# Kernel optimization log

Measured on AMD Instinct MI355X. Metric: run time of the kernel, lower is better.

## Reference

```python
import jax, jax.numpy as jnp
import numpy as np
from jax import lax

DIM = 64        # Branch(dim)
OUT = 2048      # TimesBlock out_channels == TTT model_dim
NH = 8          # num_heads
HD = OUT // NH  # 256 head dim
INNER = 4 * HD  # ttt_mlp hidden
MB = 10         # mini_batch_size
BASE_LR = 0.1   # ttt_base_lr
NK = 6          # TimesBlock num_kernels (k = 1,3,5,7,9,11)
LN_EPS = 1e-6


def _gelu(x):
    return jax.nn.gelu(x, approximate=False)


def _gelu_bwd(x):
    return 0.5 * (1.0 + lax.erf(x / jnp.sqrt(2.0))) + x * jnp.exp(-0.5 * x * x) / jnp.sqrt(2.0 * jnp.pi)


def _ttt_head(qs, ks, vs, W1h, b1h, W2h, b2h, gw, gb):
    # qs/ks/vs: [NC, MB, HD]; sequential scan over mini-batch chunks (TTT inner GD)
    eta = BASE_LR / MB

    def step(carry, chunk):
        W1c, b1c, W2c, b2c = carry
        xq, xk, xv = chunk
        Z1 = xk @ W1c + b1c              # [MB, INNER]
        A1 = _gelu(Z1)
        Z2 = A1 @ W2c + b2c              # [MB, HD]
        # grad of 0.5*||LN(Z2) - (xv - xk)||^2 wrt Z2 (fused LN l2 backward)
        tgt = xv - xk
        mu = Z2.mean(-1, keepdims=True)
        std = jnp.sqrt(Z2.var(-1, keepdims=True) + LN_EPS)
        xhat = (2 * 0 + Z2 - mu) / std
        gout = (gw * xhat + gb) - tgt
        gxh = gout * gw
        gZ2 = (gxh - gxh.mean(-1, keepdims=True) - xhat * (gxh * xhat).mean(-1, keepdims=True)) / std
        gZ1 = (gZ2 @ W2c.T) * _gelu_bwd(Z1)
        # inner-model SGD step
        W1n = W1c - eta * (xk.T @ gZ1)
        b1n = b1c - eta * gZ1.sum(0)
        W2n = W2c - eta * (A1.T @ gZ2)
        b2n = b2c - eta * gZ2.sum(0)
        # apply updated inner model to queries, post-LN + residual
        Z1q = xq @ W1n + b1n
        Z2q = _gelu(Z1q) @ W2n + b2n
        muq = Z2q.mean(-1, keepdims=True)
        stdq = jnp.sqrt(Z2q.var(-1, keepdims=True) + LN_EPS)
        out = xq + gw * ((Z2q - muq) / stdq) + gb
        return (W1n, b1n, W2n, b2n), out

    _, outs = lax.scan(step, (W1h, b1h, W2h, b2h), (qs, ks, vs))
    return outs.reshape(-1, HD)  # [T, HD]


def _forward(x, seg, conv_ws, conv_bs, wq, wk, wv, wo, W1, b1, W2, b2, ln_w, ln_b):
    B, T, C = x.shape
    xg = jnp.transpose(x, (0, 2, 1)).reshape(B, C, T // seg, seg)
    dn = ('NCHW', 'OIHW', 'NCHW')
    acc = 0.0
    for w, bc in zip(conv_ws, conv_bs):
        acc = acc + lax.conv_general_dilated(xg, w, (1, 1), 'SAME', dimension_numbers=dn) + bc[None, :, None, None]
    xb = acc / float(len(conv_ws))            # TimesBlock: mean over kernel ensemble
    xb = jax.nn.silu(xb)
    xb = jnp.transpose(xb.reshape(B, OUT, T), (0, 2, 1))  # [B, T, OUT]

    def heads(h):  # [B,T,OUT] -> [B,NH,NC,MB,HD]
        return jnp.transpose(h.reshape(B, T, NH, HD), (0, 2, 1, 3)).reshape(B, NH, T // MB, MB, HD)

    q = heads(xb @ wq.T)
    k = heads(xb @ wk.T)
    v = heads(xb @ wv.T)
    f = jax.vmap(jax.vmap(_ttt_head, in_axes=(0, 0, 0, 0, 0, 0, 0, 0, 0)),
                 in_axes=(0, 0, 0, None, None, None, None, None, None))
    o = f(q, k, v, W1, b1, W2, b2, ln_w, ln_b)  # [B, NH, T, HD]
    o = jnp.transpose(o, (0, 2, 1, 3)).reshape(B, T, OUT)
    return o @ wo.T


def setup_inputs() -> dict:
    key = jax.random.key(0)
    ks = jax.random.split(key, 24)
    B, T = 2, 400
    inp = {"x": jax.random.normal(ks[0], (B, T, DIM), jnp.float32), "seg": 20}
    for i in range(NK):
        kk = 2 * i + 1
        fan_out = OUT * kk * kk
        inp[f"conv_w{i}"] = jax.random.normal(ks[1 + i], (OUT, DIM, kk, kk), jnp.float32) * np.sqrt(2.0 / fan_out)
        inp[f"conv_b{i}"] = jnp.zeros((OUT,), jnp.float32)
    for j, nm in enumerate(["wq", "wk", "wv", "wo"]):
        inp[nm] = jax.random.normal(ks[8 + j], (OUT, OUT), jnp.float32) * 0.02
    inp["W1"] = jax.random.normal(ks[12], (NH, HD, INNER), jnp.float32) * 0.02
    inp["b1"] = jnp.zeros((NH, INNER), jnp.float32)
    inp["W2"] = jax.random.normal(ks[13], (NH, INNER, HD), jnp.float32) * 0.02
    inp["b2"] = jnp.zeros((NH, HD), jnp.float32)
    inp["ln_w"] = jnp.ones((NH, HD), jnp.float32)
    inp["ln_b"] = jnp.zeros((NH, HD), jnp.float32)
    return inp


def reference(x, seg, conv_w0, conv_b0, conv_w1, conv_b1, conv_w2, conv_b2,
              conv_w3, conv_b3, conv_w4, conv_b4, conv_w5, conv_b5,
              wq, wk, wv, wo, W1, b1, W2, b2, ln_w, ln_b):
    conv_ws = [conv_w0, conv_w1, conv_w2, conv_w3, conv_w4, conv_w5]
    conv_bs = [conv_b0, conv_b1, conv_b2, conv_b3, conv_b4, conv_b5]
    return _forward(x, seg, conv_ws, conv_bs, wq, wk, wv, wo, W1, b1, W2, b2, ln_w, ln_b)
```

## Files before the change

kernel.cpp:

```cpp
#include <hip/hip_runtime.h>


typedef __bf16 bf16x8 __attribute__((ext_vector_type(8)));
typedef float  f32x4  __attribute__((ext_vector_type(4)));

__device__ __forceinline__ unsigned short f2bf(float f){
  unsigned int u = __builtin_bit_cast(unsigned int, f);
  u += 0x7fffu + ((u >> 16) & 1u);
  return (unsigned short)(u >> 16);
}
__device__ __forceinline__ float bf2f(unsigned short b){
  unsigned int u = ((unsigned int)b) << 16;
  return __builtin_bit_cast(float, u);
}
__device__ __forceinline__ float gelu_f(float x){
  return 0.5f * x * (1.0f + erff(x * 0.70710678118654752f));
}
__device__ __forceinline__ float gelu_bwd_f(float x){
  return 0.5f * (1.0f + erff(x * 0.70710678118654752f))
       + x * __expf(-0.5f * x * x) * 0.3989422804014327f;
}

__device__ __forceinline__ float2 aload2(const float* p){
  unsigned long long v = __hip_atomic_load((const unsigned long long*)p,
                                           __ATOMIC_RELAXED, __HIP_MEMORY_SCOPE_AGENT);
  union { unsigned long long u; float2 f; } cv; cv.u = v; return cv.f;
}
__device__ __forceinline__ void aadd(float* p, float v){
  __hip_atomic_fetch_add(p, v, __ATOMIC_RELAXED, __HIP_MEMORY_SCOPE_AGENT);
}


__global__ __launch_bounds__(256) void k_weff(
    const float* __restrict__ w0, const float* __restrict__ w1,
    const float* __restrict__ w2, const float* __restrict__ w3,
    const float* __restrict__ w4, const float* __restrict__ w5,
    unsigned short* __restrict__ weff)
{
  extern __shared__ float sw[];
  const int off[6] = {0, 64, 640, 2240, 5376, 10560};
  const float* ws6[6] = {w0, w1, w2, w3, w4, w5};
  int o = blockIdx.x, tid = threadIdx.x;
#pragma unroll
  for (int i = 0; i < 6; i++){
    int kk = 2 * i + 1, sz = 64 * kk * kk;
    const float* src = ws6[i] + (size_t)o * sz;
    for (int idx = tid; idx < sz; idx += 256) sw[off[i] + idx] = src[idx];
  }
  __syncthreads();
  for (int t = tid; t < 7744; t += 256){
    int c = t / 121, dd = t % 121, di = dd / 11, dj = dd % 11;
    float s = 0.f;
#pragma unroll
    for (int i = 0; i < 6; i++){
      int kk = 2 * i + 1;
      int a = di - 5 + i, b = dj - 5 + i;
      if (a >= 0 && a < kk && b >= 0 && b < kk)
        s += sw[off[i] + (c * kk + a) * kk + b];
    }
    weff[(size_t)o * 7744 + t] = f2bf(s);
  }
}

__global__ __launch_bounds__(256) void k_im2col(
    const float* __restrict__ x, unsigned short* __restrict__ P)
{
  int idx = blockIdx.x * 256 + threadIdx.x;
  if (idx >= 800 * 7744) return;
  int n = idx / 7744, k = idx % 7744;
  int c = k / 121, dd = k % 121, di = dd / 11, dj = dd % 11;
  int b = n / 400, pos = n % 400, i = pos / 20, j = pos % 20;
  int ii = i + di - 5, jj = j + dj - 5;
  float v = 0.f;
  if (ii >= 0 && ii < 20 && jj >= 0 && jj < 20)
    v = x[((size_t)b * 400 + ii * 20 + jj) * 64 + c];
  P[idx] = f2bf(v);
}

__global__ __launch_bounds__(256) void k_wqkv(
    const float* __restrict__ wq, const float* __restrict__ wk,
    const float* __restrict__ wv, unsigned short* __restrict__ dst)
{
  int idx = blockIdx.x * 256 + threadIdx.x;
  if (idx >= 6144 * 2048) return;
  int m = idx >> 11, kk = idx & 2047;
  const float* src = (m < 2048) ? wq : ((m < 4096) ? wk : wv);
  dst[idx] = f2bf(src[(size_t)(m & 2047) * 2048 + kk]);
}

__global__ __launch_bounds__(256) void k_f2bf_copy(
    const float* __restrict__ src, unsigned short* __restrict__ dst, int n)
{
  int idx = blockIdx.x * 256 + threadIdx.x;
  if (idx < n) dst[idx] = f2bf(src[idx]);
}

__global__ __launch_bounds__(256) void k_bsum(
    const float* __restrict__ b0, const float* __restrict__ b1,
    const float* __restrict__ b2, const float* __restrict__ b3,
    const float* __restrict__ b4, const float* __restrict__ b5,
    float* __restrict__ bsum)
{
  int idx = blockIdx.x * 256 + threadIdx.x;
  if (idx < 2048)
    bsum[idx] = b0[idx] + b1[idx] + b2[idx] + b3[idx] + b4[idx] + b5[idx];
}

__global__ __launch_bounds__(256) void k_comb_silu(
    const float* __restrict__ p0, const float* __restrict__ p1,
    const float* __restrict__ bsum, unsigned short* __restrict__ xb)
{
  int i4 = (blockIdx.x * 256 + threadIdx.x) * 4;
  float4 a = *(const float4*)&p0[i4];
  float4 b = *(const float4*)&p1[i4];
  int mm = i4 & 2047;
  float4 bs = *(const float4*)&bsum[mm];
  float v[4] = {a.x + b.x + bs.x, a.y + b.y + bs.y, a.z + b.z + bs.z, a.w + b.w + bs.w};
  ushort4 o;
#pragma unroll
  for (int i = 0; i < 4; i++){
    float t = v[i] * (1.0f / 6.0f);
    float sv = t / (1.0f + __expf(-t));
    ((unsigned short*)&o)[i] = f2bf(sv);
  }
  *(ushort4*)&xb[i4] = o;
}

__global__ __launch_bounds__(256) void k_comb_add(
    const float* __restrict__ p0, const float* __restrict__ p1,
    float* __restrict__ out)
{
  int i4 = (blockIdx.x * 256 + threadIdx.x) * 4;
  float4 a = *(const float4*)&p0[i4];
  float4 b = *(const float4*)&p1[i4];
  float4 o = {a.x + b.x, a.y + b.y, a.z + b.z, a.w + b.w};
  *(float4*)&out[i4] = o;
}

template<int MODE>
__global__ __launch_bounds__(256, 1) void k_gemm(
    const unsigned short* __restrict__ A, const unsigned short* __restrict__ B,
    int M, int N, int lda, int ldb, int kLen,
    unsigned short* __restrict__ qb, unsigned short* __restrict__ kb,
    unsigned short* __restrict__ vb, float* __restrict__ outf)
{
  __shared__ unsigned short As[128 * 32];
  __shared__ unsigned short Bs[128 * 32];
  int tid = threadIdx.x, w = tid >> 6, l = tid & 63, qd = l >> 4, lm = l & 15;
  int m0 = blockIdx.x * 128, n0 = blockIdx.y * 128;
  int kBase = blockIdx.z * kLen;

  f32x4 acc[4][4];
#pragma unroll
  for (int i = 0; i < 4; i++)
#pragma unroll
    for (int j = 0; j < 4; j++){ acc[i][j][0]=0.f; acc[i][j][1]=0.f; acc[i][j][2]=0.f; acc[i][j][3]=0.f; }

  int nk = kLen >> 5;
  for (int kt = 0; kt < nk; kt++){
    int k0 = kBase + (kt << 5);
#pragma unroll
    for (int i = 0; i < 2; i++){
      int cidx = tid + i * 256;
      int row = cidx >> 2, kc = (cidx & 3) << 3;
      *(uint4*)&As[row * 32 + kc] = *(const uint4*)&A[(size_t)(m0 + row) * lda + k0 + kc];
      int br = n0 + row; if (br >= N) br = N - 1;
      *(uint4*)&Bs[row * 32 + kc] = *(const uint4*)&B[(size_t)br * ldb + k0 + kc];
    }
    __syncthreads();
    bf16x8 af[4], bfv[4];
#pragma unroll
    for (int i = 0; i < 4; i++)
      af[i] = *(const bf16x8*)&As[((w >> 1) * 64 + i * 16 + lm) * 32 + qd * 8];
#pragma unroll
    for (int j = 0; j < 4; j++)
      bfv[j] = *(const bf16x8*)&Bs[((w & 1) * 64 + j * 16 + lm) * 32 + qd * 8];
#pragma unroll
    for (int i = 0; i < 4; i++)
#pragma unroll
      for (int j = 0; j < 4; j++)
        acc[i][j] = __builtin_amdgcn_mfma_f32_16x16x32_bf16(af[i], bfv[j], acc[i][j], 0, 0, 0);
    __syncthreads();
  }

#pragma unroll
  for (int i = 0; i < 4; i++){
    int mBase = m0 + (w >> 1) * 64 + i * 16 + qd * 4;
#pragma unroll
    for (int j = 0; j < 4; j++){
      int n = n0 + (w & 1) * 64 + j * 16 + lm;
      if (n < N){
#pragma unroll
        for (int rr = 0; rr < 4; rr++){
          float val = acc[i][j][rr];
          int mm = mBase + rr;
          if (MODE == 1){
            int proj = mm >> 11, o = mm & 2047, hh = o >> 8, d = o & 255;
            int bh = (n / 400) * 8 + hh, tt = n % 400;
            unsigned short* dst = (proj == 0) ? qb : ((proj == 1) ? kb : vb);
            dst[((size_t)bh * 400 + tt) * 256 + d] = f2bf(val);
          } else {
            outf[(size_t)blockIdx.z * M * N + (size_t)n * M + mm] = val;
          }
        }
      }
    }
  }
}

#define O_W1BT 0
#define O_W2K  16896
#define O_W2N  33792
#define O_XKQ  52224
#define O_TGT  54864
#define O_A1   57424
#define O_A1T  58144
#define O_GZ2  60704
#define O_GZ1  63344
#define O_XQ2  65392
#define O_GZ2T 68032
#define O_XKT  74176
#define O_F32  80320
#define O_GW   80960
#define O_GB   81216
#define US_TOTAL 81472
#define TTT_LDS_BYTES (81472 * 2)

#define ETA 0.01f
#define BAR_STRIDE 32

__global__ __launch_bounds__(256, 1) void k_ttt(
    const unsigned short* __restrict__ qg, const unsigned short* __restrict__ kg,
    const unsigned short* __restrict__ vg,
    const float* __restrict__ W1g, const float* __restrict__ b1g,
    const float* __restrict__ W2g, const float* __restrict__ b2g,
    const float* __restrict__ gwg, const float* __restrict__ gbg,
    float* __restrict__ z2acc, unsigned short* __restrict__ zqp,
    unsigned int* __restrict__ bar)
{
  extern __shared__ unsigned short lds[];
  float* ldsf = (float*)&lds[O_F32];

  int tid = threadIdx.x, w = tid >> 6, l = tid & 63, qd = l >> 4, lm = l & 15;
  int bid = blockIdx.x;
  int jj = bid >> 3, xx = bid & 7;
  int h  = xx + 8 * (jj >> 4);
  int sl = jj & 15;
  int hh = h & 7;

  for (int i = tid; i < US_TOTAL; i += 256) lds[i] = 0;
  __syncthreads();

  float w1r[4][4][4];
#pragma unroll
  for (int a = 0; a < 4; a++)
#pragma unroll
    for (int nt = 0; nt < 4; nt++)
#pragma unroll
      for (int rr = 0; rr < 4; rr++)
        w1r[a][nt][rr] = W1g[((size_t)hh * 256 + (4 * w + a) * 16 + qd * 4 + rr) * 1024
                             + sl * 64 + nt * 16 + lm];
  float w2r[16][4];
#pragma unroll
  for (int nt = 0; nt < 16; nt++)
#pragma unroll
    for (int rr = 0; rr < 4; rr++)
      w2r[nt][rr] = W2g[((size_t)hh * 1024 + sl * 64 + w * 16 + qd * 4 + rr) * 256
                        + nt * 16 + lm];
  if (tid < 64)  ldsf[tid] = b1g[hh * 1024 + sl * 64 + tid];
  if (tid < 256){
    ldsf[64 + tid] = b2g[hh * 256 + tid];
    lds[O_GW + tid] = f2bf(gwg[hh * 256 + tid]);
    lds[O_GB + tid] = f2bf(gbg[hh * 256 + tid]);
  }

#define WRITE_W1BF() do { \
  _Pragma("unroll") for (int a = 0; a < 4; a++){ \
    int m0i = (4 * w + a) * 16 + qd * 4; \
    _Pragma("unroll") for (int nt = 0; nt < 4; nt++){ \
      int n = nt * 16 + lm; \
      unsigned int p0 = f2bf(w1r[a][nt][0]) | ((unsigned int)f2bf(w1r[a][nt][1]) << 16); \
      unsigned int p1 = f2bf(w1r[a][nt][2]) | ((unsigned int)f2bf(w1r[a][nt][3]) << 16); \
      *(unsigned int*)&lds[O_W1BT + n * 264 + m0i]     = p0; \
      *(unsigned int*)&lds[O_W1BT + n * 264 + m0i + 2] = p1; \
    } } } while(0)

#define WRITE_W2BF() do { \
  int mB = w * 16 + qd * 4; \
  _Pragma("unroll") for (int nt = 0; nt < 16; nt++){ \
    int n = nt * 16 + lm; \
    _Pragma("unroll") for (int rr = 0; rr < 4; rr++) \
      lds[O_W2K + (mB + rr) * 264 + n] = f2bf(w2r[nt][rr]); \
    unsigned int p0 = f2bf(w2r[nt][0]) | ((unsigned int)f2bf(w2r[nt][1]) << 16); \
    unsigned int p1 = f2bf(w2r[nt][2]) | ((unsigned int)f2bf(w2r[nt][3]) << 16); \
    *(unsigned int*)&lds[O_W2N + n * 72 + mB]     = p0; \
    *(unsigned int*)&lds[O_W2N + n * 72 + mB + 2] = p1; \
  } } while(0)

  const size_t hb2 = (size_t)h * 400 * 256;

#define LOAD_XK_TGT(NCH) do { \
  const unsigned int* kp = (const unsigned int*)(kg + hb2 + (size_t)(NCH) * 2560); \
  const unsigned int* vp = (const unsigned int*)(vg + hb2 + (size_t)(NCH) * 2560); \
  _Pragma("unroll") for (int i5 = 0; i5 < 5; i5++){ \
    int f2i = i5 * 256 + tid; \
    unsigned int ku = kp[f2i], vu = vp[f2i]; \
    int row = f2i >> 7, col = (f2i & 127) * 2; \
    *(unsigned int*)&lds[O_XKQ + row * 264 + col] = ku; \
    lds[O_XKT + col * 24 + row]       = (unsigned short)(ku & 0xffffu); \
    lds[O_XKT + (col + 1) * 24 + row] = (unsigned short)(ku >> 16); \
    float kv0 = bf2f((unsigned short)(ku & 0xffffu)), kv1 = bf2f((unsigned short)(ku >> 16)); \
    float vv0 = bf2f((unsigned short)(vu & 0xffffu)), vv1 = bf2f((unsigned short)(vu >> 16)); \
    unsigned int tu = (unsigned int)f2bf(vv0 - kv0) | ((unsigned int)f2bf(vv1 - kv1) << 16); \
    *(unsigned int*)&lds[O_TGT + row * 256 + col] = tu; \
  } } while(0)

  WRITE_W1BF();
  WRITE_W2BF();
  LOAD_XK_TGT(0);
  __syncthreads();

  for (int nch = 0; nch < 40; nch++){
    const size_t chunkBase = (size_t)(h * 40 + nch) * 10 * 256;

    f32x4 z1a; z1a[0]=0.f; z1a[1]=0.f; z1a[2]=0.f; z1a[3]=0.f;
#pragma unroll
    for (int ks = 0; ks < 8; ks++){
      bf16x8 av = *(const bf16x8*)&lds[O_XKQ + lm * 264 + ks * 32 + qd * 8];
      bf16x8 bv = *(const bf16x8*)&lds[O_W1BT + (w * 16 + lm) * 264 + ks * 32 + qd * 8];
      z1a = __builtin_amdgcn_mfma_f32_16x16x32_bf16(av, bv, z1a, 0, 0, 0);
    }
    float z1v[4];
    {
      float b1n = ldsf[w * 16 + lm];
#pragma unroll
      for (int rr = 0; rr < 4; rr++){
        z1v[rr] = z1a[rr] + b1n;
        int mr = qd * 4 + rr;
        if (mr < 10){
          float a1 = gelu_f(z1v[rr]);
          unsigned short ab = f2bf(a1);
          lds[O_A1 + mr * 72 + w * 16 + lm] = ab;
          lds[O_A1T + (w * 16 + lm) * 40 + mr] = ab;
        }
      }
    }
    __syncthreads();

#pragma unroll
    for (int nt4 = 0; nt4 < 4; nt4++){
      int nt = 4 * w + nt4;
      f32x4 p; p[0]=0.f; p[1]=0.f; p[2]=0.f; p[3]=0.f;
#pragma unroll
      for (int ks = 0; ks < 2; ks++){
        bf16x8 av = *(const bf16x8*)&lds[O_A1 + lm * 72 + ks * 32 + qd * 8];
        bf16x8 bv = *(const bf16x8*)&lds[O_W2N + (nt * 16 + lm) * 72 + ks * 32 + qd * 8];
        p = __builtin_amdgcn_mfma_f32_16x16x32_bf16(av, bv, p, 0, 0, 0);
      }
#pragma unroll
      for (int rr = 0; rr < 4; rr++){
        int mr = qd * 4 + rr;
        if (mr < 10)
          aadd(&z2acc[chunkBase + (size_t)mr * 256 + nt * 16 + lm], p[rr]);
      }
    }

    {
      const unsigned int* qp = (const unsigned int*)(qg + hb2 + (size_t)nch * 2560);
#pragma unroll
      for (int i5 = 0; i5 < 5; i5++){
        int f2i = i5 * 256 + tid;
        unsigned int qu = qp[f2i];
        int row = f2i >> 7, col = (f2i & 127) * 2;
        *(unsigned int*)&lds[O_XQ2 + row * 264 + col] = qu;
      }
    }

    __syncthreads();
    if (tid == 0){
      __hip_atomic_fetch_add(bar + h * BAR_STRIDE, 1u, __ATOMIC_RELAXED, __HIP_MEMORY_SCOPE_AGENT);
      unsigned int target = 16u * (unsigned int)(nch + 1);
      unsigned int spins = 0;
      while (__hip_atomic_load(bar + h * BAR_STRIDE, __ATOMIC_RELAXED, __HIP_MEMORY_SCOPE_AGENT) < target
             && spins < 8000000u){ spins++; __builtin_amdgcn_s_sleep(1); }
    }
    __syncthreads();

    for (int r2 = w; r2 < 10; r2 += 4){
      int c0 = l * 4;
      const float* bp = &z2acc[chunkBase + (size_t)r2 * 256 + c0];
      float2 u01 = aload2(bp);
      float2 u23 = aload2(bp + 2);
      float zz[4] = {u01.x, u01.y, u23.x, u23.y};
      float s1 = 0.f, s2 = 0.f;
#pragma unroll
      for (int i = 0; i < 4; i++){ zz[i] += ldsf[64 + c0 + i]; s1 += zz[i]; s2 += zz[i] * zz[i]; }
#pragma unroll
      for (int off = 32; off >= 1; off >>= 1){ s1 += __shfl_xor(s1, off, 64); s2 += __shfl_xor(s2, off, 64); }
      float mu = s1 * (1.f / 256.f);
      float var = s2 * (1.f / 256.f) - mu * mu;
      float rstd = rsqrtf(var + 1e-6f);
      float xh[4], gx[4];
      float t1 = 0.f, t2 = 0.f;
#pragma unroll
      for (int i = 0; i < 4; i++){
        xh[i] = (zz[i] - mu) * rstd;
        float gwv = bf2f(lds[O_GW + c0 + i]), gbv = bf2f(lds[O_GB + c0 + i]);
        float tg = bf2f(lds[O_TGT + r2 * 256 + c0 + i]);
        float go = gwv * xh[i] + gbv - tg;
        gx[i] = go * gwv;
        t1 += gx[i]; t2 += gx[i] * xh[i];
      }
#pragma unroll
      for (int off = 32; off >= 1; off >>= 1){ t1 += __shfl_xor(t1, off, 64); t2 += __shfl_xor(t2, off, 64); }
      float m1 = t1 * (1.f / 256.f), m2 = t2 * (1.f / 256.f);
      float g0 = (gx[0] - m1 - xh[0] * m2) * rstd;
      float g1 = (gx[1] - m1 - xh[1] * m2) * rstd;
      float g2 = (gx[2] - m1 - xh[2] * m2) * rstd;
      float g3 = (gx[3] - m1 - xh[3] * m2) * rstd;
      unsigned int p0 = f2bf(g0) | ((unsigned int)f2bf(g1) << 16);
      unsigned int p1 = f2bf(g2) | ((unsigned int)f2bf(g3) << 16);
      *(unsigned int*)&lds[O_GZ2 + r2 * 264 + c0]     = p0;
      *(unsigned int*)&lds[O_GZ2 + r2 * 264 + c0 + 2] = p1;
    }
    __syncthreads();

    {
      float sum = 0.f;
#pragma unroll
      for (int r2 = 0; r2 < 10; r2++){
        unsigned short g = lds[O_GZ2 + r2 * 264 + tid];
        lds[O_GZ2T + tid * 24 + r2] = g;
        sum += bf2f(g);
      }
      ldsf[64 + tid] -= ETA * sum;
    }
    {
      f32x4 g1a; g1a[0]=0.f; g1a[1]=0.f; g1a[2]=0.f; g1a[3]=0.f;
#pragma unroll
      for (int ks = 0; ks < 8; ks++){
        bf16x8 av = *(const bf16x8*)&lds[O_GZ2 + lm * 264 + ks * 32 + qd * 8];
        bf16x8 bv = *(const bf16x8*)&lds[O_W2K + (w * 16 + lm) * 264 + ks * 32 + qd * 8];
        g1a = __builtin_amdgcn_mfma_f32_16x16x32_bf16(av, bv, g1a, 0, 0, 0);
      }
#pragma unroll
      for (int rr = 0; rr < 4; rr++){
        int mr = qd * 4 + rr;
        if (mr < 10){
          float gz1 = g1a[rr] * gelu_bwd_f(z1v[rr]);
          lds[O_GZ1 + (w * 16 + lm) * 32 + mr] = f2bf(gz1);
        }
      }
    }
    __syncthreads();

    if (tid < 64){
      float sum = 0.f;
#pragma unroll
      for (int kx = 0; kx < 10; kx++) sum += bf2f(lds[O_GZ1 + tid * 32 + kx]);
      ldsf[tid] -= ETA * sum;
    }
#pragma unroll
    for (int a = 0; a < 4; a++){
      int mt = 4 * w + a;
      bf16x8 av = *(const bf16x8*)&lds[O_XKT + (mt * 16 + lm) * 24 + (qd & 1) * 8];
#pragma unroll
      for (int nt = 0; nt < 4; nt++){
        bf16x8 bv = *(const bf16x8*)&lds[O_GZ1 + (nt * 16 + lm) * 32 + qd * 8];
        f32x4 d; d[0]=0.f; d[1]=0.f; d[2]=0.f; d[3]=0.f;
        d = __builtin_amdgcn_mfma_f32_16x16x32_bf16(av, bv, d, 0, 0, 0);
#pragma unroll
        for (int rr = 0; rr < 4; rr++) w1r[a][nt][rr] -= ETA * d[rr];
      }
    }
    {
      bf16x8 av2 = *(const bf16x8*)&lds[O_A1T + (w * 16 + lm) * 40 + qd * 8];
#pragma unroll
      for (int nt = 0; nt < 16; nt++){
        bf16x8 bv = *(const bf16x8*)&lds[O_GZ2T + (nt * 16 + lm) * 24 + (qd & 1) * 8];
        f32x4 d; d[0]=0.f; d[1]=0.f; d[2]=0.f; d[3]=0.f;
        d = __builtin_amdgcn_mfma_f32_16x16x32_bf16(av2, bv, d, 0, 0, 0);
#pragma unroll
        for (int rr = 0; rr < 4; rr++) w2r[nt][rr] -= ETA * d[rr];
      }
    }
    WRITE_W1BF();
    WRITE_W2BF();
    __syncthreads();

    if (nch + 1 < 40) LOAD_XK_TGT(nch + 1);

    {
      f32x4 zq; zq[0]=0.f; zq[1]=0.f; zq[2]=0.f; zq[3]=0.f;
#pragma unroll
      for (int ks = 0; ks < 8; ks++){
        bf16x8 av = *(const bf16x8*)&lds[O_XQ2 + lm * 264 + ks * 32 + qd * 8];
        bf16x8 bv = *(const bf16x8*)&lds[O_W1BT + (w * 16 + lm) * 264 + ks * 32 + qd * 8];
        zq = __builtin_amdgcn_mfma_f32_16x16x32_bf16(av, bv, zq, 0, 0, 0);
      }
      float b1n = ldsf[w * 16 + lm];
#pragma unroll
      for (int rr = 0; rr < 4; rr++){
        int mr = qd * 4 + rr;
        if (mr < 10)
          lds[O_A1 + mr * 72 + w * 16 + lm] = f2bf(gelu_f(zq[rr] + b1n));
      }
    }
    __syncthreads();

    {
      unsigned short* zq_out = zqp + ((size_t)(h * 16 + sl) * 40 + nch) * 2560;
#pragma unroll
      for (int nt4 = 0; nt4 < 4; nt4++){
        int nt = 4 * w + nt4;
        f32x4 p; p[0]=0.f; p[1]=0.f; p[2]=0.f; p[3]=0.f;
#pragma unroll
        for (int ks = 0; ks < 2; ks++){
          bf16x8 av = *(const bf16x8*)&lds[O_A1 + lm * 72 + ks * 32 + qd * 8];
          bf16x8 bv = *(const bf16x8*)&lds[O_W2N + (nt * 16 + lm) * 72 + ks * 32 + qd * 8];
          p = __builtin_amdgcn_mfma_f32_16x16x32_bf16(av, bv, p, 0, 0, 0);
        }
        float bb = (sl == 0) ? ldsf[64 + nt * 16 + lm] : 0.f;
#pragma unroll
        for (int rr = 0; rr < 4; rr++){
          int mr = qd * 4 + rr;
          if (mr < 10)
            zq_out[mr * 256 + nt * 16 + lm] = f2bf(p[rr] + bb);
        }
      }
    }
    __syncthreads();
  }
}

__global__ __launch_bounds__(256) void k_lnout(
    const unsigned short* __restrict__ zqp, const unsigned short* __restrict__ qg,
    const float* __restrict__ gwg, const float* __restrict__ gbg,
    unsigned short* __restrict__ obf)
{
  int w = threadIdx.x >> 6, l = threadIdx.x & 63;
  int gr = blockIdx.x * 4 + w;
  int h = gr / 400, t = gr % 400, hh = h & 7, b = h >> 3;
  int nch = t / 10, mr = t % 10;
  int c0 = l * 4;
  float z[4] = {0.f, 0.f, 0.f, 0.f};
#pragma unroll
  for (int sl = 0; sl < 16; sl++){
    const unsigned short* zp = zqp + (((size_t)(h * 16 + sl) * 40 + nch) * 10 + mr) * 256 + c0;
    ushort4 u = *(const ushort4*)zp;
    z[0] += bf2f(u.x); z[1] += bf2f(u.y); z[2] += bf2f(u.z); z[3] += bf2f(u.w);
  }
  float s1 = 0.f, s2 = 0.f;
#pragma unroll
  for (int i = 0; i < 4; i++){ s1 += z[i]; s2 += z[i] * z[i]; }
#pragma unroll
  for (int off = 32; off >= 1; off >>= 1){ s1 += __shfl_xor(s1, off, 64); s2 += __shfl_xor(s2, off, 64); }
  float mu = s1 * (1.f / 256.f);
  float var = s2 * (1.f / 256.f) - mu * mu;
  float rstd = rsqrtf(var + 1e-6f);
  const unsigned short* qp = &qg[((size_t)h * 400 + t) * 256];
  ushort4 qu = *(const ushort4*)&qp[c0];
  float qv[4] = {bf2f(qu.x), bf2f(qu.y), bf2f(qu.z), bf2f(qu.w)};
  unsigned short* op = &obf[((size_t)(b * 400 + t)) * 2048 + hh * 256];
#pragma unroll
  for (int i = 0; i < 4; i++){
    float xh = (z[i] - mu) * rstd;
    float o = qv[i] + gwg[hh * 256 + c0 + i] * xh + gbg[hh * 256 + c0 + i];
    op[c0 + i] = f2bf(o);
  }
}

#define WS_WEFF   0u
#define WS_P      31719424u
#define WS_WQKV   44109824u
#define WS_WOB    52428800u
#define WS_Z2ACC  62722048u
#define WS_XB     69275648u
#define WS_Q      72552448u
#define WS_K      75829248u
#define WS_V      79106048u
#define WS_OBF    82382848u
#define WS_BSUM   85659648u
#define WS_BAR    85667840u

extern "C" void kernel_launch(void* const* d_in, const int* in_sizes, int n_in,
                              void* d_out, int out_size, void* d_ws, size_t ws_size,
                              hipStream_t stream)
{
  (void)in_sizes; (void)n_in; (void)out_size; (void)ws_size;
  const float* x  = (const float*)d_in[0];
  const float* cw[6]; const float* cb[6];
  for (int i = 0; i < 6; i++){ cw[i] = (const float*)d_in[2 + 2 * i]; cb[i] = (const float*)d_in[3 + 2 * i]; }
  const float* wq  = (const float*)d_in[14];
  const float* wk  = (const float*)d_in[15];
  const float* wv  = (const float*)d_in[16];
  const float* wo  = (const float*)d_in[17];
  const float* W1  = (const float*)d_in[18];
  const float* b1  = (const float*)d_in[19];
  const float* W2  = (const float*)d_in[20];
  const float* b2  = (const float*)d_in[21];
  const float* lnw = (const float*)d_in[22];
  const float* lnb = (const float*)d_in[23];
  float* outf = (float*)d_out;

  char* wsb = (char*)d_ws;
  unsigned short* weff = (unsigned short*)(wsb + WS_WEFF);
  unsigned short* P    = (unsigned short*)(wsb + WS_P);
  unsigned short* wqkv = (unsigned short*)(wsb + WS_WQKV);
  unsigned short* wob  = (unsigned short*)(wsb + WS_WOB);
  unsigned short* xb   = (unsigned short*)(wsb + WS_XB);
  unsigned short* qb   = (unsigned short*)(wsb + WS_Q);
  unsigned short* kb   = (unsigned short*)(wsb + WS_K);
  unsigned short* vb   = (unsigned short*)(wsb + WS_V);
  float* z2acc = (float*)(wsb + WS_Z2ACC);
  unsigned short* zqp = (unsigned short*)(wsb + WS_WEFF);
  unsigned short* obf = (unsigned short*)(wsb + WS_OBF);
  float* bsum = (float*)(wsb + WS_BSUM);
  unsigned int* bar = (unsigned int*)(wsb + WS_BAR);
  float* g0part = (float*)(wsb + WS_Q);
  float* g2part = (float*)(wsb + WS_Z2ACC);

  hipMemsetAsync(bar, 0, 16 * BAR_STRIDE * 4, stream);
  hipFuncSetAttribute(reinterpret_cast<const void*>(k_ttt),
                      hipFuncAttributeMaxDynamicSharedMemorySize, TTT_LDS_BYTES);
  hipFuncSetAttribute(reinterpret_cast<const void*>(k_weff),
                      hipFuncAttributeMaxDynamicSharedMemorySize, 18304 * 4);

  k_weff<<<2048, 256, 18304 * 4, stream>>>(cw[0], cw[1], cw[2], cw[3], cw[4], cw[5], weff);
  k_im2col<<<(800 * 7744 + 255) / 256, 256, 0, stream>>>(x, P);
  k_wqkv<<<(6144 * 2048 + 255) / 256, 256, 0, stream>>>(wq, wk, wv, wqkv);
  k_bsum<<<8, 256, 0, stream>>>(cb[0], cb[1], cb[2], cb[3], cb[4], cb[5], bsum);

  k_gemm<2><<<dim3(16, 7, 2), 256, 0, stream>>>(weff, P, 2048, 800, 7744, 7744, 3872,
                                                nullptr, nullptr, nullptr, g0part);
  k_comb_silu<<<1600, 256, 0, stream>>>(g0part, g0part + 1638400, bsum, xb);

  k_gemm<1><<<dim3(48, 7, 1), 256, 0, stream>>>(wqkv, xb, 6144, 800, 2048, 2048, 2048,
                                                qb, kb, vb, nullptr);

  k_f2bf_copy<<<(2048 * 2048 + 255) / 256, 256, 0, stream>>>(wo, wob, 2048 * 2048);
  hipMemsetAsync(z2acc, 0, 16 * 40 * 10 * 256 * 4, stream);

  k_ttt<<<256, 256, TTT_LDS_BYTES, stream>>>(qb, kb, vb, W1, b1, W2, b2, lnw, lnb,
                                             z2acc, zqp, bar);
  k_lnout<<<1600, 256, 0, stream>>>(zqp, qb, lnw, lnb, obf);

  k_gemm<2><<<dim3(16, 7, 2), 256, 0, stream>>>(wob, obf, 2048, 800, 2048, 2048, 1024,
                                                nullptr, nullptr, nullptr, g2part);
  k_comb_add<<<1600, 256, 0, stream>>>(g2part, g2part + 1638400, outf);
}
```

Baseline: 1.130 ms.

## Overlap deferred query output with cross-block barrier wait; split output GEMM four-way

In the TTT kernel, the query-path output for chunk n-1 (Z1q, GELU and the Z2q MFMA plus the global store) now runs after the barrier arrive and before the spin-wait for chunk n. The wait latency is hidden behind useful work, and the query load for the next chunk is prefetched in the same window, with a tail step after the loop for the last chunk. The A1T LDS stride is shrunk and a separate A1Q buffer is added. The output projection GEMM uses a 4-way K split instead of 2-way for more blocks, and its partials go to a larger workspace region combined by a 4-input add kernel. The risks are extra partial-sum traffic and correctness of the reordered synchronisation.

```diff
diff --git a/kernel.cpp b/kernel.cpp
--- a/kernel.cpp
+++ b/kernel.cpp
@@ -126,14 +126,16 @@
   *(ushort4*)&xb[i4] = o;
 }
 
-__global__ __launch_bounds__(256) void k_comb_add(
-    const float* __restrict__ p0, const float* __restrict__ p1,
-    float* __restrict__ out)
+__global__ __launch_bounds__(256) void k_comb_add4(
+    const float* __restrict__ p, float* __restrict__ out)
 {
   int i4 = (blockIdx.x * 256 + threadIdx.x) * 4;
-  float4 a = *(const float4*)&p0[i4];
-  float4 b = *(const float4*)&p1[i4];
-  float4 o = {a.x + b.x, a.y + b.y, a.z + b.z, a.w + b.w};
+  float4 a = *(const float4*)&p[i4];
+  float4 b = *(const float4*)&p[1638400 + i4];
+  float4 c = *(const float4*)&p[3276800 + i4];
+  float4 d = *(const float4*)&p[4915200 + i4];
+  float4 o = {a.x + b.x + c.x + d.x, a.y + b.y + c.y + d.y,
+              a.z + b.z + c.z + d.z, a.w + b.w + c.w + d.w};
   *(float4*)&out[i4] = o;
 }
 
@@ -215,16 +217,17 @@
 #define O_TGT  54864
 #define O_A1   57424
 #define O_A1T  58144
-#define O_GZ2  60704
-#define O_GZ1  63344
-#define O_XQ2  65392
-#define O_GZ2T 68032
-#define O_XKT  74176
-#define O_F32  80320
-#define O_GW   80960
-#define O_GB   81216
-#define US_TOTAL 81472
-#define TTT_LDS_BYTES (81472 * 2)
+#define O_GZ2  60192
+#define O_GZ1  62832
+#define O_XQ2  64880
+#define O_GZ2T 67520
+#define O_XKT  73664
+#define O_A1Q  79808
+#define O_F32  80528
+#define O_GW   81168
+#define O_GB   81424
+#define US_TOTAL 81680
+#define TTT_LDS_BYTES (81680 * 2)
 
 #define ETA 0.01f
 #define BAR_STRIDE 32
@@ -315,9 +318,19 @@
     *(unsigned int*)&lds[O_TGT + row * 256 + col] = tu; \
   } } while(0)
 
+#define LOAD_XQ(NCH) do { \
+  const unsigned int* qp = (const unsigned int*)(qg + hb2 + (size_t)(NCH) * 2560); \
+  _Pragma("unroll") for (int i5 = 0; i5 < 5; i5++){ \
+    int f2i = i5 * 256 + tid; \
+    unsigned int qu = qp[f2i]; \
+    int row = f2i >> 7, col = (f2i & 127) * 2; \
+    *(unsigned int*)&lds[O_XQ2 + row * 264 + col] = qu; \
+  } } while(0)
+
   WRITE_W1BF();
   WRITE_W2BF();
   LOAD_XK_TGT(0);
+  LOAD_XQ(0);
   __syncthreads();
 
   for (int nch = 0; nch < 40; nch++){
@@ -341,7 +354,7 @@
           float a1 = gelu_f(z1v[rr]);
           unsigned short ab = f2bf(a1);
           lds[O_A1 + mr * 72 + w * 16 + lm] = ab;
-          lds[O_A1T + (w * 16 + lm) * 40 + mr] = ab;
+          lds[O_A1T + (w * 16 + lm) * 32 + mr] = ab;
         }
       }
     }
@@ -364,21 +377,53 @@
           aadd(&z2acc[chunkBase + (size_t)mr * 256 + nt * 16 + lm], p[rr]);
       }
     }
-
-    {
-      const unsigned int* qp = (const unsigned int*)(qg + hb2 + (size_t)nch * 2560);
-#pragma unroll
-      for (int i5 = 0; i5 < 5; i5++){
-        int f2i = i5 * 256 + tid;
-        unsigned int qu = qp[f2i];
-        int row = f2i >> 7, col = (f2i & 127) * 2;
-        *(unsigned int*)&lds[O_XQ2 + row * 264 + col] = qu;
-      }
-    }
-
-    __syncthreads();
+    __syncthreads();
+
+    if (tid == 0)
+      __hip_atomic_fetch_add(bar + h * BAR_STRIDE, 1u, __ATOMIC_RELAXED, __HIP_MEMORY_SCOPE_AGENT);
+
+    if (nch > 0){
+      f32x4 zq; zq[0]=0.f; zq[1]=0.f; zq[2]=0.f; zq[3]=0.f;
+#pragma unroll
+      for (int ks = 0; ks < 8; ks++){
+        bf16x8 av = *(const bf16x8*)&lds[O_XQ2 + lm * 264 + ks * 32 + qd * 8];
+        bf16x8 bv = *(const bf16x8*)&lds[O_W1BT + (w * 16 + lm) * 264 + ks * 32 + qd * 8];
+        zq = __builtin_amdgcn_mfma_f32_16x16x32_bf16(av, bv, zq, 0, 0, 0);
+      }
+      float b1n = ldsf[w * 16 + lm];
+#pragma unroll
+      for (int rr = 0; rr < 4; rr++){
+        int mr = qd * 4 + rr;
+        if (mr < 10)
+          lds[O_A1Q + mr * 72 + w * 16 + lm] = f2bf(gelu_f(zq[rr] + b1n));
+      }
+    }
+    __syncthreads();
+
+    if (nch > 0){
+      LOAD_XQ(nch);
+      unsigned short* zq_out = zqp + ((size_t)(h * 16 + sl) * 40 + (nch - 1)) * 2560;
+#pragma unroll
+      for (int nt4 = 0; nt4 < 4; nt4++){
+        int nt = 4 * w + nt4;
+        f32x4 p; p[0]=0.f; p[1]=0.f; p[2]=0.f; p[3]=0.f;
+#pragma unroll
+        for (int ks = 0; ks < 2; ks++){
+          bf16x8 av = *(const bf16x8*)&lds[O_A1Q + lm * 72 + ks * 32 + qd * 8];
+          bf16x8 bv = *(const bf16x8*)&lds[O_W2N + (nt * 16 + lm) * 72 + ks * 32 + qd * 8];
+          p = __builtin_amdgcn_mfma_f32_16x16x32_bf16(av, bv, p, 0, 0, 0);
+        }
+        float bb = (sl == 0) ? ldsf[64 + nt * 16 + lm] : 0.f;
+#pragma unroll
+        for (int rr = 0; rr < 4; rr++){
+          int mr = qd * 4 + rr;
+          if (mr < 10)
+            zq_out[mr * 256 + nt * 16 + lm] = f2bf(p[rr] + bb);
+        }
+      }
+    }
+
     if (tid == 0){
-      __hip_atomic_fetch_add(bar + h * BAR_STRIDE, 1u, __ATOMIC_RELAXED, __HIP_MEMORY_SCOPE_AGENT);
       unsigned int target = 16u * (unsigned int)(nch + 1);
       unsigned int spins = 0;
       while (__hip_atomic_load(bar + h * BAR_STRIDE, __ATOMIC_RELAXED, __HIP_MEMORY_SCOPE_AGENT) < target
@@ -474,7 +519,7 @@
       }
     }
     {
-      bf16x8 av2 = *(const bf16x8*)&lds[O_A1T + (w * 16 + lm) * 40 + qd * 8];
+      bf16x8 av2 = *(const bf16x8*)&lds[O_A1T + (w * 16 + lm) * 32 + qd * 8];
 #pragma unroll
       for (int nt = 0; nt < 16; nt++){
         bf16x8 bv = *(const bf16x8*)&lds[O_GZ2T + (nt * 16 + lm) * 24 + (qd & 1) * 8];
@@ -488,48 +533,49 @@
     WRITE_W2BF();
     __syncthreads();
 
-    if (nch + 1 < 40) LOAD_XK_TGT(nch + 1);
-
-    {
-      f32x4 zq; zq[0]=0.f; zq[1]=0.f; zq[2]=0.f; zq[3]=0.f;
-#pragma unroll
-      for (int ks = 0; ks < 8; ks++){
-        bf16x8 av = *(const bf16x8*)&lds[O_XQ2 + lm * 264 + ks * 32 + qd * 8];
-        bf16x8 bv = *(const bf16x8*)&lds[O_W1BT + (w * 16 + lm) * 264 + ks * 32 + qd * 8];
-        zq = __builtin_amdgcn_mfma_f32_16x16x32_bf16(av, bv, zq, 0, 0, 0);
-      }
-      float b1n = ldsf[w * 16 + lm];
+    if (nch + 1 < 40){
+      LOAD_XK_TGT(nch + 1);
+    }
+    __syncthreads();
+  }
+
+  {
+    f32x4 zq; zq[0]=0.f; zq[1]=0.f; zq[2]=0.f; zq[3]=0.f;
+#pragma unroll
+    for (int ks = 0; ks < 8; ks++){
+      bf16x8 av = *(const bf16x8*)&lds[O_XQ2 + lm * 264 + ks * 32 + qd * 8];
+      bf16x8 bv = *(const bf16x8*)&lds[O_W1BT + (w * 16 + lm) * 264 + ks * 32 + qd * 8];
+      zq = __builtin_amdgcn_mfma_f32_16x16x32_bf16(av, bv, zq, 0, 0, 0);
+    }
+    float b1n = ldsf[w * 16 + lm];
+#pragma unroll
+    for (int rr = 0; rr < 4; rr++){
+      int mr = qd * 4 + rr;
+      if (mr < 10)
+        lds[O_A1Q + mr * 72 + w * 16 + lm] = f2bf(gelu_f(zq[rr] + b1n));
+    }
+  }
+  __syncthreads();
+  {
+    unsigned short* zq_out = zqp + ((size_t)(h * 16 + sl) * 40 + 39) * 2560;
+#pragma unroll
+    for (int nt4 = 0; nt4 < 4; nt4++){
+      int nt = 4 * w + nt4;
+      f32x4 p; p[0]=0.f; p[1]=0.f; p[2]=0.f; p[3]=0.f;
+#pragma unroll
+      for (int ks = 0; ks < 2; ks++){
+        bf16x8 av = *(const bf16x8*)&lds[O_A1Q + lm * 72 + ks * 32 + qd * 8];
+        bf16x8 bv = *(const bf16x8*)&lds[O_W2N + (nt * 16 + lm) * 72 + ks * 32 + qd * 8];
+        p = __builtin_amdgcn_mfma_f32_16x16x32_bf16(av, bv, p, 0, 0, 0);
+      }
+      float bb = (sl == 0) ? ldsf[64 + nt * 16 + lm] : 0.f;
 #pragma unroll
       for (int rr = 0; rr < 4; rr++){
         int mr = qd * 4 + rr;
         if (mr < 10)
-          lds[O_A1 + mr * 72 + w * 16 + lm] = f2bf(gelu_f(zq[rr] + b1n));
-      }
-    }
-    __syncthreads();
-
-    {
-      unsigned short* zq_out = zqp + ((size_t)(h * 16 + sl) * 40 + nch) * 2560;
-#pragma unroll
-      for (int nt4 = 0; nt4 < 4; nt4++){
-        int nt = 4 * w + nt4;
-        f32x4 p; p[0]=0.f; p[1]=0.f; p[2]=0.f; p[3]=0.f;
-#pragma unroll
-        for (int ks = 0; ks < 2; ks++){
-          bf16x8 av = *(const bf16x8*)&lds[O_A1 + lm * 72 + ks * 32 + qd * 8];
-          bf16x8 bv = *(const bf16x8*)&lds[O_W2N + (nt * 16 + lm) * 72 + ks * 32 + qd * 8];
-          p = __builtin_amdgcn_mfma_f32_16x16x32_bf16(av, bv, p, 0, 0, 0);
-        }
-        float bb = (sl == 0) ? ldsf[64 + nt * 16 + lm] : 0.f;
-#pragma unroll
-        for (int rr = 0; rr < 4; rr++){
-          int mr = qd * 4 + rr;
-          if (mr < 10)
-            zq_out[mr * 256 + nt * 16 + lm] = f2bf(p[rr] + bb);
-        }
-      }
-    }
-    __syncthreads();
+          zq_out[mr * 256 + nt * 16 + lm] = f2bf(p[rr] + bb);
+      }
+    }
   }
 }
 
@@ -618,7 +664,7 @@
   float* bsum = (float*)(wsb + WS_BSUM);
   unsigned int* bar = (unsigned int*)(wsb + WS_BAR);
   float* g0part = (float*)(wsb + WS_Q);
-  float* g2part = (float*)(wsb + WS_Z2ACC);
+  float* g2part = (float*)(wsb + WS_WEFF);
 
   hipMemsetAsync(bar, 0, 16 * BAR_STRIDE * 4, stream);
   hipFuncSetAttribute(reinterpret_cast<const void*>(k_ttt),
@@ -645,7 +691,7 @@
                                              z2acc, zqp, bar);
   k_lnout<<<1600, 256, 0, stream>>>(zqp, qb, lnw, lnb, obf);
 
-  k_gemm<2><<<dim3(16, 7, 2), 256, 0, stream>>>(wob, obf, 2048, 800, 2048, 2048, 1024,
+  k_gemm<2><<<dim3(16, 7, 4), 256, 0, stream>>>(wob, obf, 2048, 800, 2048, 2048, 512,
                                                 nullptr, nullptr, nullptr, g2part);
-  k_comb_add<<<1600, 256, 0, stream>>>(g2part, g2part + 1638400, outf);
-}
+  k_comb_add4<<<1600, 256, 0, stream>>>(g2part, outf);
+}
```

New measurement: 1.101 ms. -2.6%, faster.
